# Performance work log

Hardware: AMD Instinct MI355X
Metric: run time of the kernel (lower is better)

## Reference

```python
import jax, jax.numpy as jnp
import numpy as np

B, S, E, H = 4, 1024, 1024, 16
D = E // H  # 64


def setup_inputs() -> dict:
    key = jax.random.key(0)
    ks = jax.random.split(key, 11)
    scale = 1.0 / np.sqrt(E)
    inp = {
        "q": jax.random.normal(ks[0], (B, S, E), jnp.float32),
        "k": jax.random.normal(ks[1], (B, S, E), jnp.float32),
        "v": jax.random.normal(ks[2], (B, S, E), jnp.float32),
        "mask": jax.random.randint(ks[3], (B, 1, 1, S), 0, 2, jnp.int32),
        # torch.nn.Linear params: W is [out, in], y = x @ W.T + b
        "Wq": jax.random.uniform(ks[4], (E, E), jnp.float32, -scale, scale),
        "bq": jax.random.uniform(ks[5], (E,), jnp.float32, -scale, scale),
        "Wk": jax.random.uniform(ks[6], (E, E), jnp.float32, -scale, scale),
        "bk": jax.random.uniform(ks[7], (E,), jnp.float32, -scale, scale),
        "Wo": jax.random.uniform(ks[8], (E, E), jnp.float32, -scale, scale),
        "bo": jax.random.uniform(ks[9], (E,), jnp.float32, -scale, scale),
    }
    return inp


def reference(q, k, v, mask, Wq, bq, Wk, bk, Wo, bo):
    # Projections. NOTE: original code applies key_linear to v (value_linear unused).
    qh = (q @ Wq.T + bq).reshape(B, S, H, D).transpose(0, 2, 1, 3)  # [B,H,S,D]
    kh = (k @ Wk.T + bk).reshape(B, S, H, D).transpose(0, 2, 1, 3)
    vh = (v @ Wk.T + bk).reshape(B, S, H, D).transpose(0, 2, 1, 3)

    scores = jnp.einsum("bhqd,bhkd->bhqk", qh, kh) / jnp.sqrt(jnp.float32(D))
    pad = mask == 0  # [B,1,1,S] broadcast
    scores = jnp.where(pad, jnp.float32(-1e9), scores)
    attn = jax.nn.softmax(scores, axis=-1)
    attn = jnp.where(pad, jnp.float32(0.0), attn)

    ctx = jnp.einsum("bhqk,bhkd->bhqd", attn, vh)  # [B,H,S,D]
    ctx = ctx.transpose(0, 2, 1, 3).reshape(B, S, E)
    return ctx @ Wo.T + bo
```

## Files before the change

### kernel.cpp

```cpp
#include <hip/hip_runtime.h>

typedef unsigned short u16;
typedef unsigned int   u32;
typedef __attribute__((ext_vector_type(8))) short bf16x8;
typedef __attribute__((ext_vector_type(4))) float f32x4;
typedef __attribute__((ext_vector_type(4))) u32   u32x4;

#define MFMA(a,b,c) __builtin_amdgcn_mfma_f32_16x16x32_bf16(a,b,c,0,0,0)


__device__ __forceinline__ u32 cvtpk(float lo, float hi){
  u32 r; asm("v_cvt_pk_bf16_f32 %0, %1, %2" : "=v"(r) : "v"(lo), "v"(hi)); return r;
}
__device__ __forceinline__ u16 f2bf(float f){ return (u16)cvtpk(f,f); }
__device__ __forceinline__ bf16x8 cvt8(f32x4 lo, f32x4 hi){
  u32x4 u;
  u.x = cvtpk(lo[0],lo[1]); u.y = cvtpk(lo[2],lo[3]);
  u.z = cvtpk(hi[0],hi[1]); u.w = cvtpk(hi[2],hi[3]);
  return *(bf16x8*)&u;
}

__device__ __forceinline__ int swz(int row, int col){
  return (((row<<6) + col)<<1) ^ ((row&7)<<4);
}

__device__ __forceinline__ void gl16(const void* g, void* l){
  __builtin_amdgcn_global_load_lds(
      (const __attribute__((address_space(1))) u32*)g,
      (__attribute__((address_space(3))) u32*)l, 16, 0, 0);
}

template<int ROWS>
__device__ __forceinline__ void stage_bf16(const u16* g, size_t ldg, char* lds, int wv, int lane){
  #pragma unroll
  for (int i=0;i<ROWS/32;++i){
    const int r0 = wv*(ROWS/4) + (i<<3);
    const int row = r0 + (lane>>3);
    const int c = ((lane&7) ^ (row&7)) << 3;
    gl16(g + (size_t)row*ldg + c, lds + (r0<<7));
  }
}

__device__ __forceinline__ bf16x8 frag_bf16(const char* lds, int row, int kcol){
  return *(const bf16x8*)(lds + swz(row,kcol));
}

__global__ __launch_bounds__(256) void prep_k(
    const float* __restrict__ wq, const float* __restrict__ wk, const float* __restrict__ wo,
    const float* __restrict__ q,  const float* __restrict__ k,  const float* __restrict__ v,
    u16* __restrict__ out,
    const int* __restrict__ mask, int* __restrict__ gidx, int* __restrict__ cnts)
{
  const int tid = threadIdx.x;
  if (blockIdx.x < 7680){
    const size_t i8 = (((size_t)blockIdx.x<<8) + tid) << 3;
    const float* src;
    if      (i8 <  1048576u) src = wq + i8;
    else if (i8 <  2097152u) src = wk + (i8 - 1048576u);
    else if (i8 <  3145728u) src = wo + (i8 - 2097152u);
    else if (i8 <  7340032u) src = q  + (i8 - 3145728u);
    else if (i8 < 11534336u){
      const size_t off = i8 - 7340032u;
      if (!mask[off>>10]) return;
      src = k + off;
    } else {
      const size_t off = i8 - 11534336u;
      if (!mask[off>>10]) return;
      src = v + off;
    }
    f32x4 lo = *(const f32x4*)src, hi = *(const f32x4*)(src+4);
    *(bf16x8*)(out + i8) = cvt8(lo, hi);
  } else {
    const int b = blockIdx.x - 7680, lane = tid&63, wv = tid>>6;
    __shared__ int wsum[4];
    int4 z4; z4.x=0; z4.y=0; z4.z=0; z4.w=0;
    *(int4*)(gidx + (b<<10) + (tid<<2)) = z4;
    const int4 m = *(const int4*)(mask + (b<<10) + (tid<<2));
    const int c0 = (m.x!=0)+(m.y!=0)+(m.z!=0)+(m.w!=0);
    int pre = c0;
    #pragma unroll
    for (int i=1;i<64;i<<=1){
      int t = __shfl_up(pre, i);
      if (lane >= i) pre += t;
    }
    if (lane==63) wsum[wv] = pre;
    __syncthreads();
    int base = pre - c0;
    #pragma unroll
    for (int w=0;w<4;++w) if (w<wv) base += wsum[w];
    int p = base;
    const int s0 = tid<<2;
    if (m.x) gidx[(b<<10) + p++] = s0;
    if (m.y) gidx[(b<<10) + p++] = s0+1;
    if (m.z) gidx[(b<<10) + p++] = s0+2;
    if (m.w) gidx[(b<<10) + p++] = s0+3;
    if (tid==255) cnts[b] = p;
  }
}

template<int V, bool GA, bool GB>
__device__ __forceinline__ void proj_body(
    const u16* __restrict__ Aa, const u16* __restrict__ Bb,
    const int* __restrict__ gA, const int* __restrict__ gB,
    const float* __restrict__ bias, u16* __restrict__ outb,
    char* As, char* Bs)
{
  const int tid = threadIdx.x, lane = tid&63, wv = tid>>6;
  const int wm = wv>>1, wn = wv&1, l15 = lane&15, g4 = lane>>4;

  int growA[4], growB[4];
  if (GA){
    #pragma unroll
    for (int i=0;i<4;++i) growA[i] = gA[(wv<<5)+(i<<3)+(lane>>3)] & 1023;
  }
  if (GB){
    #pragma unroll
    for (int i=0;i<4;++i) growB[i] = gB[(wv<<5)+(i<<3)+(lane>>3)] & 1023;
  }

  f32x4 acc[4][4] = {};

  #pragma unroll 1
  for (int kt=0; kt<1024; kt+=64){
    __syncthreads();
    #pragma unroll
    for (int i=0;i<4;++i){
      const int r0 = (wv<<5)+(i<<3), row = r0+(lane>>3);
      const int c = ((lane&7)^(row&7))<<3;
      const u16* srcA = GA ? Aa + (size_t)growA[i]*1024 + kt + c
                           : Aa + (size_t)row*1024 + kt + c;
      gl16(srcA, As + (r0<<7));
      const u16* srcB = GB ? Bb + (size_t)growB[i]*1024 + kt + c
                           : Bb + (size_t)row*1024 + kt + c;
      gl16(srcB, Bs + (r0<<7));
    }
    __syncthreads();

    #pragma unroll
    for (int kb=0;kb<64;kb+=32){
      const int kcol = kb + (g4<<3);
      bf16x8 af[4], bf_[4];
      #pragma unroll
      for (int t=0;t<4;++t)
        af[t] = frag_bf16(As, (wm<<6) + (t<<4) + l15, kcol);
      #pragma unroll
      for (int t=0;t<4;++t)
        bf_[t] = frag_bf16(Bs, (wn<<6) + (t<<4) + l15, kcol);
      #pragma unroll
      for (int mt=0;mt<4;++mt)
        #pragma unroll
        for (int nt=0;nt<4;++nt)
          acc[mt][nt] = MFMA(af[mt], bf_[nt], acc[mt][nt]);
    }
  }

  f32x4 bmv[4];
  if (V==1){
    #pragma unroll
    for (int mt=0;mt<4;++mt)
      bmv[mt] = *(const f32x4*)(bias + (wm<<6) + (mt<<4) + (g4<<2));
  }
  #pragma unroll
  for (int nt=0;nt<4;++nt){
    const int col = (wn<<6) + (nt<<4) + l15;
    const float bvn = (V==1) ? 0.f : bias[col];
    #pragma unroll
    for (int mt=0;mt<4;++mt){
      f32x4 a = acc[mt][nt];
      #pragma unroll
      for (int j=0;j<4;++j){
        const int ml = (wm<<6) + (mt<<4) + (g4<<2) + j;
        const float val = a[j] + ((V==1) ? bmv[mt][j] : bvn);
        if (V==1) outb[(size_t)ml*4096 + col] = f2bf(val);
        else      outb[(size_t)ml*1024 + col] = f2bf(val);
      }
    }
  }
}

__global__ __launch_bounds__(256,4) void proj_k(
    const u16* __restrict__ qb, const u16* __restrict__ kb, const u16* __restrict__ vb,
    const u16* __restrict__ wqb, const u16* __restrict__ wkb,
    const float* __restrict__ bq, const float* __restrict__ bk,
    u16* __restrict__ qp, u16* __restrict__ kp, u16* __restrict__ vt,
    const int* __restrict__ gidx, const int* __restrict__ cnts)
{
  __shared__ __align__(16) char As[16384];
  __shared__ __align__(16) char Bs[16384];
  const int bid = blockIdx.x;
  if (bid < 256){
    const int m0 = (bid&31)<<7, n0 = ((bid>>5)&7)<<7;
    proj_body<0,false,false>(qb + (size_t)m0*1024, wqb + (size_t)n0*1024, nullptr, nullptr,
                             bq + n0, qp + (size_t)m0*1024 + n0, As, Bs);
  } else if (bid < 512){
    const int local = bid-256;
    const int m0 = (local&31)<<7, n0 = ((local>>5)&7)<<7;
    const int b = m0>>10, mloc = m0&1023;
    if (mloc >= cnts[b]) return;
    proj_body<0,true,false>(kb + ((size_t)(b<<10))*1024, wkb + (size_t)n0*1024,
                            gidx + (b<<10) + mloc, nullptr,
                            bk + n0, kp + ((size_t)((b<<10)+mloc))*1024 + n0, As, Bs);
  } else {
    const int local = bid-512;
    const int m0 = (local&7)<<7, n0 = (local>>3)<<7;
    const int b = n0>>10, nloc = n0&1023;
    if (nloc >= cnts[b]) return;
    proj_body<1,false,true>(wkb + (size_t)m0*1024, vb + ((size_t)(b<<10))*1024,
                            nullptr, gidx + (b<<10) + nloc,
                            bk + m0, vt + (size_t)m0*4096 + (b<<10) + nloc, As, Bs);
  }
}

__global__ __launch_bounds__(256,4) void oproj_k(
    const u16* __restrict__ ctx, const u16* __restrict__ wob,
    const float* __restrict__ bo, float* __restrict__ of)
{
  constexpr int BN = 64, NT = 2;
  __shared__ __align__(16) char As[16384];
  __shared__ __align__(16) char Bs[BN*128];
  const int m0 = blockIdx.x<<7, n0 = blockIdx.y*BN;
  const int tid = threadIdx.x, lane = tid&63, wv = tid>>6;
  const int wm = wv>>1, wn = wv&1, l15 = lane&15, g4 = lane>>4;

  f32x4 acc[4][NT] = {};

  #pragma unroll 1
  for (int kt=0; kt<1024; kt+=64){
    __syncthreads();
    stage_bf16<128>(ctx + (size_t)m0*1024 + kt, 1024, As, wv, lane);
    stage_bf16<BN> (wob + (size_t)n0*1024 + kt, 1024, Bs, wv, lane);
    __syncthreads();

    #pragma unroll
    for (int kb=0;kb<64;kb+=32){
      const int kcol = kb + (g4<<3);
      bf16x8 af[4], bf_[NT];
      #pragma unroll
      for (int t=0;t<4;++t)
        af[t] = frag_bf16(As, (wm<<6) + (t<<4) + l15, kcol);
      #pragma unroll
      for (int t=0;t<NT;++t)
        bf_[t] = frag_bf16(Bs, wn*(BN>>1) + (t<<4) + l15, kcol);
      #pragma unroll
      for (int mt=0;mt<4;++mt)
        #pragma unroll
        for (int nt=0;nt<NT;++nt)
          acc[mt][nt] = MFMA(af[mt], bf_[nt], acc[mt][nt]);
    }
  }

  #pragma unroll
  for (int nt=0;nt<NT;++nt){
    const int col = n0 + wn*(BN>>1) + (nt<<4) + l15;
    const float bvn = bo[col];
    #pragma unroll
    for (int mt=0;mt<4;++mt){
      const int mb = m0 + (wm<<6) + (mt<<4) + (g4<<2);
      f32x4 a = acc[mt][nt];
      #pragma unroll
      for (int j=0;j<4;++j)
        of[(size_t)(mb+j)*1024 + col] = a[j] + bvn;
    }
  }
}

__global__ __launch_bounds__(256) void attn_k(
    const u16* __restrict__ qp, const u16* __restrict__ kp, const u16* __restrict__ vt,
    const int* __restrict__ cnts, u16* __restrict__ ctx)
{
  const int bid = blockIdx.x;
  const int wg  = (bid&7)*64 + (bid>>3);
  const int qt = wg&7, h = (wg>>3)&15, b = wg>>7;

  __shared__ __align__(16) u16 Qs[128*64];
  __shared__ __align__(16) u16 Ks[64*64];
  __shared__ __align__(16) u16 Vs[64*64];
  __shared__ __align__(16) u16 Ps[4*32*64];

  const int tid = threadIdx.x, lane = tid&63, wv = tid>>6;
  const int hc = h<<6, l15 = lane&15;
  const float C2 = 0.18033688011112042f;

  const int cnt = cnts[b];
  const int ntiles = (cnt + 63) >> 6;

  {
    const u16* Qg = qp + ((size_t)((b<<10) + (qt<<7)))*1024 + hc;
    #pragma unroll
    for (int i=0;i<4;++i){
      const int r0 = (wv<<5) + (i<<3);
      const int row = r0 + (lane>>3);
      const int c = ((lane&7) ^ (row&7)) << 3;
      gl16(Qg + (size_t)row*1024 + c, (char*)Qs + (r0<<7));
    }
  }

  const u16* Kg = kp + ((size_t)(b<<10))*1024 + hc;
  const u16* Vg = vt + ((size_t)hc)*4096 + (b<<10);

  f32x4 o[2][4] = {};
  float lr[2][4] = {};
  u16* Pw = Ps + (wv<<11);

  #pragma unroll 1
  for (int kt=0; kt<ntiles; ++kt){
    __syncthreads();
    {
      #pragma unroll
      for (int i=0;i<2;++i){
        const int r0 = (wv<<4) + (i<<3);
        const int row = r0 + (lane>>3);
        const int c = ((lane&7) ^ (row&7)) << 3;
        gl16(Kg + (size_t)((kt<<6) + row)*1024 + c, (char*)Ks + (r0<<7));
        gl16(Vg + (size_t)row*4096 + (kt<<6) + c,  (char*)Vs + (r0<<7));
      }
    }
    __syncthreads();

    f32x4 sc[2][4] = {};
    #pragma unroll
    for (int kb=0;kb<64;kb+=32){
      const int kcol = kb + ((lane>>4)<<3);
      bf16x8 kf[4];
      #pragma unroll
      for (int nt=0;nt<4;++nt) kf[nt] = frag_bf16((const char*)Ks, (nt<<4)+l15, kcol);
      bf16x8 aq0 = frag_bf16((const char*)Qs, (wv<<5)+l15, kcol);
      bf16x8 aq1 = frag_bf16((const char*)Qs, (wv<<5)+16+l15, kcol);
      __builtin_amdgcn_s_setprio(1);
      #pragma unroll
      for (int nt=0;nt<4;++nt) sc[0][nt] = MFMA(aq0, kf[nt], sc[0][nt]);
      #pragma unroll
      for (int nt=0;nt<4;++nt) sc[1][nt] = MFMA(aq1, kf[nt], sc[1][nt]);
      __builtin_amdgcn_s_setprio(0);
    }

    float bv4[4];
    #pragma unroll
    for (int nt=0;nt<4;++nt)
      bv4[nt] = ((kt<<6)+(nt<<4)+l15 < cnt) ? 0.f : -1e30f;
    #pragma unroll
    for (int sub=0;sub<2;++sub)
      #pragma unroll
      for (int nt=0;nt<4;++nt){
        f32x4 s = sc[sub][nt];
        #pragma unroll
        for (int j=0;j<4;++j){
          const float p = __builtin_amdgcn_exp2f(fmaf(s[j], C2, bv4[nt]));
          lr[sub][j] += p;
          *(u16*)((char*)Pw + swz((sub<<4)+((lane>>4)<<2)+j, (nt<<4)+l15)) = f2bf(p);
        }
      }
    asm volatile("s_waitcnt lgkmcnt(0)" ::: "memory");
    __builtin_amdgcn_sched_barrier(0);

    #pragma unroll
    for (int kb=0;kb<64;kb+=32){
      const int kcol = kb + ((lane>>4)<<3);
      bf16x8 vf[4];
      #pragma unroll
      for (int nt=0;nt<4;++nt) vf[nt] = frag_bf16((const char*)Vs, (nt<<4)+l15, kcol);
      bf16x8 pa0 = frag_bf16((const char*)Pw, l15, kcol);
      bf16x8 pa1 = frag_bf16((const char*)Pw, 16+l15, kcol);
      __builtin_amdgcn_s_setprio(1);
      #pragma unroll
      for (int nt=0;nt<4;++nt) o[0][nt] = MFMA(pa0, vf[nt], o[0][nt]);
      #pragma unroll
      for (int nt=0;nt<4;++nt) o[1][nt] = MFMA(pa1, vf[nt], o[1][nt]);
      __builtin_amdgcn_s_setprio(0);
    }
  }

  #pragma unroll
  for (int sub=0;sub<2;++sub)
    #pragma unroll
    for (int j=0;j<4;++j){
      float s = lr[sub][j];
      s += __shfl_xor(s,1); s += __shfl_xor(s,2);
      s += __shfl_xor(s,4); s += __shfl_xor(s,8);
      const float inv = 1.f / fmaxf(s, 1e-30f);
      const int row = (qt<<7) + (wv<<5) + (sub<<4) + ((lane>>4)<<2) + j;
      u16* crow = ctx + ((size_t)((b<<10)+row))*1024 + hc;
      #pragma unroll
      for (int nt=0;nt<4;++nt)
        crow[(nt<<4)+l15] = f2bf(o[sub][nt][j]*inv);
    }
}

extern "C" void kernel_launch(void* const* d_in, const int* in_sizes, int n_in,
                              void* d_out, int out_size, void* d_ws, size_t ws_size,
                              hipStream_t stream) {
  const float* q    = (const float*)d_in[0];
  const float* k    = (const float*)d_in[1];
  const float* v    = (const float*)d_in[2];
  const int*   mask = (const int*)  d_in[3];
  const float* Wq   = (const float*)d_in[4];
  const float* bq   = (const float*)d_in[5];
  const float* Wk   = (const float*)d_in[6];
  const float* bk   = (const float*)d_in[7];
  const float* Wo   = (const float*)d_in[8];
  const float* bo   = (const float*)d_in[9];
  float* out = (float*)d_out;

  char* ws = (char*)d_ws;
  u16* wqb  = (u16*)(ws);
  u16* wkb  = (u16*)(ws +  2097152);
  u16* wob  = (u16*)(ws +  4194304);
  u16* qb   = (u16*)(ws +  6291456);
  u16* kb   = (u16*)(ws + 14680064);
  u16* vb   = (u16*)(ws + 23068672);
  u16* qp   = (u16*)(ws + 31457280);
  u16* kp   = (u16*)(ws + 39845888);
  u16* vtb  = (u16*)(ws + 48234496);
  u16* ctxb = (u16*)(ws + 56623104);
  int* gidx = (int*)(ws + 65011712);
  int* cnts = (int*)(ws + 65028096);

  dim3 blk(256);
  prep_k<<<7684, blk, 0, stream>>>(Wq, Wk, Wo, q, k, v, wqb, mask, gidx, cnts);
  proj_k<<<768, blk, 0, stream>>>(qb, kb, vb, wqb, wkb, bq, bk, qp, kp, vtb, gidx, cnts);
  attn_k<<<512, blk, 0, stream>>>(qp, kp, vtb, cnts, ctxb);
  oproj_k<<<dim3(32,16), blk, 0, stream>>>(ctxb, wob, bo, out);
}
```

Baseline: 81.51 us.

## Double-buffer LDS tiles in projection GEMM to overlap loads with MFMA

The projection GEMM body now uses two LDS buffers for the A and B tiles. It issues the global-to-LDS loads for the next K tile before running the MFMAs on the current one, leaving one barrier per iteration instead of two. The aim is to hide global memory latency behind compute. This doubles LDS use to 64KB per block and lowers the occupancy hint in launch bounds from 4 to 2 blocks per CU, which costs latency hiding across waves.

Result: slower. 90.79 us (+11.4%).

```diff
diff --git a/kernel.cpp b/kernel.cpp
--- a/kernel.cpp
+++ b/kernel.cpp
@@ -103,38 +103,40 @@
     const u16* __restrict__ Aa, const u16* __restrict__ Bb,
     const int* __restrict__ gA, const int* __restrict__ gB,
     const float* __restrict__ bias, u16* __restrict__ outb,
-    char* As, char* Bs)
+    char* As0, char* Bs0)
 {
   const int tid = threadIdx.x, lane = tid&63, wv = tid>>6;
   const int wm = wv>>1, wn = wv&1, l15 = lane&15, g4 = lane>>4;
 
   int growA[4], growB[4];
-  if (GA){
-    #pragma unroll
-    for (int i=0;i<4;++i) growA[i] = gA[(wv<<5)+(i<<3)+(lane>>3)] & 1023;
-  }
-  if (GB){
-    #pragma unroll
-    for (int i=0;i<4;++i) growB[i] = gB[(wv<<5)+(i<<3)+(lane>>3)] & 1023;
-  }
-
-  f32x4 acc[4][4] = {};
-
-  #pragma unroll 1
-  for (int kt=0; kt<1024; kt+=64){
-    __syncthreads();
+  #pragma unroll
+  for (int i=0;i<4;++i){
+    const int row = (wv<<5)+(i<<3)+(lane>>3);
+    growA[i] = GA ? (gA[row] & 1023) : row;
+    growB[i] = GB ? (gB[row] & 1023) : row;
+  }
+
+  auto stageAB = [&](int kt, char* Ad, char* Bd){
     #pragma unroll
     for (int i=0;i<4;++i){
       const int r0 = (wv<<5)+(i<<3), row = r0+(lane>>3);
       const int c = ((lane&7)^(row&7))<<3;
-      const u16* srcA = GA ? Aa + (size_t)growA[i]*1024 + kt + c
-                           : Aa + (size_t)row*1024 + kt + c;
-      gl16(srcA, As + (r0<<7));
-      const u16* srcB = GB ? Bb + (size_t)growB[i]*1024 + kt + c
-                           : Bb + (size_t)row*1024 + kt + c;
-      gl16(srcB, Bs + (r0<<7));
-    }
-    __syncthreads();
+      gl16(Aa + (size_t)growA[i]*1024 + kt + c, Ad + (r0<<7));
+      gl16(Bb + (size_t)growB[i]*1024 + kt + c, Bd + (r0<<7));
+    }
+  };
+
+  f32x4 acc[4][4] = {};
+
+  stageAB(0, As0, Bs0);
+  __syncthreads();
+
+  int cb = 0;
+  #pragma unroll 1
+  for (int kt=0; kt<1024; kt+=64){
+    char* Ac = As0 + (cb<<14);       char* Bc = Bs0 + (cb<<14);
+    char* An = As0 + ((cb^1)<<14);   char* Bn = Bs0 + ((cb^1)<<14);
+    if (kt < 960) stageAB(kt+64, An, Bn);
 
     #pragma unroll
     for (int kb=0;kb<64;kb+=32){
@@ -142,16 +144,18 @@
       bf16x8 af[4], bf_[4];
       #pragma unroll
       for (int t=0;t<4;++t)
-        af[t] = frag_bf16(As, (wm<<6) + (t<<4) + l15, kcol);
+        af[t] = frag_bf16(Ac, (wm<<6) + (t<<4) + l15, kcol);
       #pragma unroll
       for (int t=0;t<4;++t)
-        bf_[t] = frag_bf16(Bs, (wn<<6) + (t<<4) + l15, kcol);
+        bf_[t] = frag_bf16(Bc, (wn<<6) + (t<<4) + l15, kcol);
       #pragma unroll
       for (int mt=0;mt<4;++mt)
         #pragma unroll
         for (int nt=0;nt<4;++nt)
           acc[mt][nt] = MFMA(af[mt], bf_[nt], acc[mt][nt]);
     }
+    __syncthreads();
+    cb ^= 1;
   }
 
   f32x4 bmv[4];
@@ -178,20 +182,20 @@
   }
 }
 
-__global__ __launch_bounds__(256,4) void proj_k(
+__global__ __launch_bounds__(256,2) void proj_k(
     const u16* __restrict__ qb, const u16* __restrict__ kb, const u16* __restrict__ vb,
     const u16* __restrict__ wqb, const u16* __restrict__ wkb,
     const float* __restrict__ bq, const float* __restrict__ bk,
     u16* __restrict__ qp, u16* __restrict__ kp, u16* __restrict__ vt,
     const int* __restrict__ gidx, const int* __restrict__ cnts)
 {
-  __shared__ __align__(16) char As[16384];
-  __shared__ __align__(16) char Bs[16384];
+  __shared__ __align__(16) char As[2][16384];
+  __shared__ __align__(16) char Bs[2][16384];
   const int bid = blockIdx.x;
   if (bid < 256){
     const int m0 = (bid&31)<<7, n0 = ((bid>>5)&7)<<7;
     proj_body<0,false,false>(qb + (size_t)m0*1024, wqb + (size_t)n0*1024, nullptr, nullptr,
-                             bq + n0, qp + (size_t)m0*1024 + n0, As, Bs);
+                             bq + n0, qp + (size_t)m0*1024 + n0, As[0], Bs[0]);
   } else if (bid < 512){
     const int local = bid-256;
     const int m0 = (local&31)<<7, n0 = ((local>>5)&7)<<7;
@@ -199,7 +203,7 @@
     if (mloc >= cnts[b]) return;
     proj_body<0,true,false>(kb + ((size_t)(b<<10))*1024, wkb + (size_t)n0*1024,
                             gidx + (b<<10) + mloc, nullptr,
-                            bk + n0, kp + ((size_t)((b<<10)+mloc))*1024 + n0, As, Bs);
+                            bk + n0, kp + ((size_t)((b<<10)+mloc))*1024 + n0, As[0], Bs[0]);
   } else {
     const int local = bid-512;
     const int m0 = (local&7)<<7, n0 = (local>>3)<<7;
@@ -207,7 +211,7 @@
     if (nloc >= cnts[b]) return;
     proj_body<1,false,true>(wkb + (size_t)m0*1024, vb + ((size_t)(b<<10))*1024,
                             nullptr, gidx + (b<<10) + nloc,
-                            bk + m0, vt + (size_t)m0*4096 + (b<<10) + nloc, As, Bs);
+                            bk + m0, vt + (size_t)m0*4096 + (b<<10) + nloc, As[0], Bs[0]);
   }
 }
 
```
